# Kernel tuning notes

Measured on AMD Instinct MI355X. Metric: run time of the kernel, lower is better.

## Reference

```python
import jax, jax.numpy as jnp
import numpy as np

PAD = 0
B, P, ENC = 64, 196, 2048
L, V, H, E, A = 20, 32000, 512, 512, 512


def setup_inputs() -> dict:
    key = jax.random.key(0)
    ks = jax.random.split(key, 24)
    enc_out = jax.random.normal(ks[0], (B, P, ENC), dtype=jnp.float32)
    # captions: random tokens in [3, V) with variable lengths in [5, L]; sample 0 has full length L
    lengths = jax.random.randint(ks[1], (B,), 5, L + 1)
    lengths = lengths.at[0].set(L)
    toks = jax.random.randint(ks[2], (B, L), 3, V)
    pos = jnp.arange(L)
    y = jnp.where(pos[None, :] < lengths[:, None], toks, PAD).astype(jnp.int64)
    s = lambda k, shp, sc: (jax.random.normal(k, shp, dtype=jnp.float32) * sc)
    return {
        "encoder_output": enc_out,
        "y_encodings": y,
        "embed_table": jax.random.uniform(ks[3], (V, E), minval=-0.1, maxval=0.1, dtype=jnp.float32),
        "enc2att_W": s(ks[4], (A, ENC), 0.02),
        "hidden2att_W": s(ks[5], (A, H), 0.04),
        "att_W": s(ks[6], (1, A), 0.06),
        "att_b": jnp.zeros((1,), jnp.float32),
        "f_beta_W": s(ks[7], (ENC, H), 0.03),
        "f_beta_b": jnp.zeros((ENC,), jnp.float32),
        "W_ih": s(ks[8], (4 * H, E + ENC), 0.02),
        "b_ih": jnp.zeros((4 * H,), jnp.float32),
        "W_hh": s(ks[9], (4 * H, H), 0.04),
        "b_hh": jnp.zeros((4 * H,), jnp.float32),
        "fc_W": jax.random.uniform(ks[10], (V, H), minval=-0.1, maxval=0.1, dtype=jnp.float32),
        "fc_b": jnp.zeros((V,), jnp.float32),
        "init_h_W": s(ks[11], (H, ENC), 0.03),
        "init_h_b": jnp.zeros((H,), jnp.float32),
        "init_c_W": s(ks[12], (H, ENC), 0.03),
        "init_c_b": jnp.zeros((H,), jnp.float32),
    }


def _decode(encoder_output, y_encodings, embed_table, enc2att_W, hidden2att_W,
            att_W, att_b, f_beta_W, f_beta_b, W_ih, b_ih, W_hh, b_hh,
            fc_W, fc_b, init_h_W, init_h_b, init_c_W, init_c_b):
    # sort batch by caption length (descending), as in torch
    cap_len = jnp.sum(y_encodings != PAD, axis=1)          # [B]
    sort_idx = jnp.argsort(-cap_len)                       # stable in jax
    enc = encoder_output[sort_idx]                         # [B,P,ENC]
    caps = y_encodings[sort_idx]                           # [B,L]
    dec_len = cap_len[sort_idx] - 1                        # [B]
    T = L - 1                                              # static max decode length

    embed = embed_table[caps]                              # [B,L,E]
    mean_enc = enc.mean(axis=1)                            # [B,ENC]
    h0 = mean_enc @ init_h_W.T + init_h_b
    c0 = mean_enc @ init_c_W.T + init_c_b
    att1 = jnp.einsum('bpe,ae->bpa', enc, enc2att_W)       # [B,P,A], time-invariant

    def step(carry, xs):
        h, c = carry
        emb_t, t = xs                                      # emb_t: [B,E]
        # soft attention
        att2 = h @ hidden2att_W.T                          # [B,A]
        score = jnp.einsum('bpa,a->bp', jax.nn.relu(att1 + att2[:, None, :]), att_W[0]) + att_b[0]
        alpha = jax.nn.softmax(score, axis=1)              # [B,P]
        context = jnp.einsum('bp,bpe->be', alpha, enc)     # [B,ENC]
        gate = jax.nn.sigmoid(h @ f_beta_W.T + f_beta_b)   # [B,ENC]
        ctx = gate * context
        # LSTM cell (torch gate order: i, f, g, o)
        x_in = jnp.concatenate([emb_t, ctx], axis=1)       # [B,E+ENC]
        gates = x_in @ W_ih.T + b_ih + h @ W_hh.T + b_hh   # [B,4H]
        i_g, f_g, g_g, o_g = jnp.split(gates, 4, axis=1)
        c_new = jax.nn.sigmoid(f_g) * c + jax.nn.sigmoid(i_g) * jnp.tanh(g_g)
        h_new = jax.nn.sigmoid(o_g) * jnp.tanh(c_new)
        logits = h_new @ fc_W.T + fc_b                     # [B,V]
        active = (dec_len > t)[:, None]
        h = jnp.where(active, h_new, h)
        c = jnp.where(active, c_new, c)
        preds_t = jnp.where(active, logits, 0.0)
        alpha_t = jnp.where(active, alpha, 0.0)
        return (h, c), (preds_t, alpha_t)

    xs = (jnp.swapaxes(embed, 0, 1)[:T], jnp.arange(T))
    _, (preds, alphas) = jax.lax.scan(step, (h0, c0), xs)
    predictions = jnp.swapaxes(preds, 0, 1)               # [B,T,V]
    alphas = jnp.swapaxes(alphas, 0, 1)                   # [B,T,P]
    return predictions, alphas, dec_len, sort_idx


def reference(encoder_output, y_encodings, embed_table, enc2att_W, hidden2att_W,
              att_W, att_b, f_beta_W, f_beta_b, W_ih, b_ih, W_hh, b_hh,
              fc_W, fc_b, init_h_W, init_h_b, init_c_W, init_c_b):
    return _decode(encoder_output, y_encodings, embed_table, enc2att_W, hidden2att_W,
                   att_W, att_b, f_beta_W, f_beta_b, W_ih, b_ih, W_hh, b_hh,
                   fc_W, fc_b, init_h_W, init_h_b, init_c_W, init_c_b)
```

## Files before the change

kernel.cpp:

```cpp
#include <hip/hip_runtime.h>
#include <cstdint>
#include <cstddef>

#define BB 64
#define PE 196
#define PP 208
#define ENC 2048
#define LL 20
#define TT 19
#define VV 32000
#define HH 512
#define AA 512
#define KCAT 3072
#define XROW 3072
#define MROW 1216
#define MPAD 1280

typedef __attribute__((ext_vector_type(8))) short bf16x8;
typedef __attribute__((ext_vector_type(4))) float f32x4;
typedef unsigned short u16;
typedef unsigned int u32;

__device__ __forceinline__ float bf2f(u16 s){ return __uint_as_float(((u32)s) << 16); }
__device__ __forceinline__ u16 f2bf(float f){
  u32 u = __float_as_uint(f);
  u32 r = (u + 0x7FFFu + ((u >> 16) & 1u)) >> 16;
  return (u16)r;
}
__device__ __forceinline__ f32x4 mfma16(bf16x8 a, bf16x8 b, f32x4 c){
  return __builtin_amdgcn_mfma_f32_16x16x32_bf16(a, b, c, 0, 0, 0);
}
__device__ __forceinline__ float sigm(float x){ return 1.f / (1.f + __expf(-x)); }

__device__ __forceinline__ void gl_lds16(const u16* g, u16* l){
  __builtin_amdgcn_global_load_lds(
      (const __attribute__((address_space(1))) void*)g,
      (__attribute__((address_space(3))) void*)l, 16, 0, 0);
}


__global__ void k_sort(const int* __restrict__ y, int* __restrict__ sidx, int* __restrict__ dlen,
                       float* __restrict__ out_dlen, float* __restrict__ out_sidx){
  __shared__ int cl[BB];
  int b = threadIdx.x;
  int c = 0;
  for (int l = 0; l < LL; l++) c += (y[b*LL + l] != 0);
  cl[b] = c;
  __syncthreads();
  int r = 0;
  for (int j = 0; j < BB; j++){
    int cj = cl[j];
    r += (cj > c) || (cj == c && j < b);
  }
  sidx[r] = b; dlen[r] = c - 1;
  out_sidx[r] = (float)b; out_dlen[r] = (float)(c - 1);
}

__global__ void k_cvt(u16* __restrict__ dst, const float* __restrict__ src, int n){
  int i = blockIdx.x * blockDim.x + threadIdx.x;
  int stride = gridDim.x * blockDim.x;
  for (; i < n; i += stride) dst[i] = f2bf(src[i]);
}

__global__ void k_wcat(u16* __restrict__ wcat, const float* __restrict__ wih, const float* __restrict__ whh){
  int r = blockIdx.x;
  for (int j = threadIdx.x; j < KCAT; j += 256){
    float v = (j < 2560) ? wih[(size_t)r*2560 + j] : whh[(size_t)r*HH + (j - 2560)];
    wcat[(size_t)r*KCAT + j] = f2bf(v);
  }
}

__global__ void k_gather(u16* __restrict__ encb, const float* __restrict__ enc, const int* __restrict__ sidx){
  int b = blockIdx.x, pg = blockIdx.y;
  int s = sidx[b];
  const float* src = enc + (size_t)s * PE * ENC;
  u16* dst = encb + ((size_t)b * PP + pg * 8) * ENC;
  for (int i = threadIdx.x; i < 8 * ENC; i += 256){
    int p = pg * 8 + (i >> 11);
    dst[i] = (p < PE) ? f2bf(src[(size_t)p * ENC + (i & 2047)]) : (u16)0;
  }
}

__global__ void k_mean(float* __restrict__ mean, const u16* __restrict__ encb){
  int b = blockIdx.x;
  int e = blockIdx.y * 256 + threadIdx.x;
  const u16* p = encb + (size_t)b * PP * ENC + e;
  float s = 0.f;
#pragma unroll 14
  for (int pp = 0; pp < PE; pp++) s += bf2f(p[(size_t)pp * ENC]);
  mean[b*ENC + e] = s * (1.0f / 196.0f);
}

__global__ void k_embed(u16* __restrict__ embb, const float* __restrict__ table,
                        const int* __restrict__ y, const int* __restrict__ sidx){
  int b = blockIdx.x; int s = sidx[b];
  for (int i = threadIdx.x; i < TT * HH; i += 256){
    int tt = i >> 9, j = i & 511;
    int tok = y[s*LL + tt];
    embb[((size_t)b*TT + tt)*HH + j] = f2bf(table[(size_t)tok * HH + j]);
  }
}

__global__ void k_init(u16* __restrict__ xcat, float* __restrict__ cws, const float* __restrict__ mean,
                       const float* __restrict__ hW, const float* __restrict__ hb,
                       const float* __restrict__ cW, const float* __restrict__ cb){
  int isC = blockIdx.y;
  int col = blockIdx.x * 4 + (threadIdx.x >> 6);
  int row = threadIdx.x & 63;
  const float* W = isC ? cW : hW;
  const float4* m4 = (const float4*)(mean + (size_t)row * ENC);
  const float4* w4 = (const float4*)(W + (size_t)col * ENC);
  float acc = 0.f;
#pragma unroll 8
  for (int k = 0; k < ENC/4; k++){
    float4 a = m4[k], w = w4[k];
    acc = fmaf(a.x, w.x, acc); acc = fmaf(a.y, w.y, acc);
    acc = fmaf(a.z, w.z, acc); acc = fmaf(a.w, w.w, acc);
  }
  if (isC) cws[row*HH + col] = acc + cb[col];
  else     xcat[(size_t)row*XROW + 2560 + col] = f2bf(acc + hb[col]);
}

__global__ __launch_bounds__(256, 2) void k_att1(u16* __restrict__ att1,
                                                 const u16* __restrict__ encb,
                                                 const u16* __restrict__ e2a){
  __shared__ u16 ldsA[128 * 32];
  __shared__ u16 ldsB[128 * 32];
  int tid = threadIdx.x;
  int wave = tid >> 6, lane = tid & 63, quad = lane >> 4, l15 = lane & 15, kq = quad * 8;
  int mbase = blockIdx.x * 128;
  int nbase = blockIdx.y * 128;
  int wm = (wave >> 1) * 64, wn = (wave & 1) * 64;

  int srow = tid >> 2;
  int scol = (tid & 3) * 8;
  const u16* gA0 = encb + (size_t)(mbase + srow) * ENC + scol;
  const u16* gA1 = encb + (size_t)(mbase + 64 + srow) * ENC + scol;
  const u16* gB0 = e2a  + (size_t)(nbase + srow) * ENC + scol;
  const u16* gB1 = e2a  + (size_t)(nbase + 64 + srow) * ENC + scol;
  u16* lA0 = ldsA + tid * 8;
  u16* lA1 = ldsA + 2048 + tid * 8;
  u16* lB0 = ldsB + tid * 8;
  u16* lB1 = ldsB + 2048 + tid * 8;

  f32x4 acc[4][4] = {};
  for (int k0 = 0; k0 < ENC; k0 += 32){
    gl_lds16(gA0 + k0, lA0);
    gl_lds16(gA1 + k0, lA1);
    gl_lds16(gB0 + k0, lB0);
    gl_lds16(gB1 + k0, lB1);
    __syncthreads();
    bf16x8 af[4], bfr[4];
#pragma unroll
    for (int i = 0; i < 4; i++) af[i]  = *(const bf16x8*)(ldsA + (wm + i*16 + l15) * 32 + kq);
#pragma unroll
    for (int j = 0; j < 4; j++) bfr[j] = *(const bf16x8*)(ldsB + (wn + j*16 + l15) * 32 + kq);
#pragma unroll
    for (int i = 0; i < 4; i++)
#pragma unroll
      for (int j = 0; j < 4; j++)
        acc[i][j] = mfma16(af[i], bfr[j], acc[i][j]);
    __syncthreads();
  }
#pragma unroll
  for (int i = 0; i < 4; i++)
#pragma unroll
    for (int j = 0; j < 4; j++)
#pragma unroll
      for (int r = 0; r < 4; r++){
        int m = mbase + wm + i*16 + quad*4 + r;
        int n = nbase + wn + j*16 + l15;
        att1[(size_t)m * AA + n] = f2bf(acc[i][j][r]);
      }
}


__global__ void k_hmat(float* __restrict__ att2, float* __restrict__ gatelin,
                       const u16* __restrict__ xcat, const u16* __restrict__ whcat){
  int lane = threadIdx.x, quad = lane >> 4, l15 = lane & 15, kq = quad * 8;
  int n = blockIdx.x * 16 + l15;
  const u16* bp = whcat + (size_t)n * HH + kq;
  f32x4 acc[4] = {};
#pragma unroll 4
  for (int k0 = 0; k0 < HH; k0 += 32){
    bf16x8 bv = *(const bf16x8*)(bp + k0);
#pragma unroll
    for (int mt = 0; mt < 4; mt++){
      bf16x8 av = *(const bf16x8*)(xcat + (size_t)(mt*16 + l15)*XROW + 2560 + kq + k0);
      acc[mt] = mfma16(av, bv, acc[mt]);
    }
  }
#pragma unroll
  for (int mt = 0; mt < 4; mt++)
#pragma unroll
    for (int r = 0; r < 4; r++){
      int m = mt*16 + quad*4 + r;
      float v = acc[mt][r];
      if (n < HH) att2[m*HH + n] = v;
      else        gatelin[m*ENC + (n - HH)] = v;
    }
}

__global__ void k_score(float* __restrict__ out_alph, float* __restrict__ alpha_ws,
                        const u16* __restrict__ att1, const float* __restrict__ att2,
                        const float* __restrict__ attW, const float* __restrict__ attb,
                        const int* __restrict__ dlen, int t){
  __shared__ float a2s[AA], aws[AA], red[256];
  int b = blockIdx.x, tid = threadIdx.x;
  float* oa = out_alph + ((size_t)b*TT + t) * PE;
  if (dlen[b] <= t){
    if (tid < PE) oa[tid] = 0.f;
    return;
  }
  a2s[tid] = att2[b*AA + tid]; a2s[tid+256] = att2[b*AA + tid + 256];
  aws[tid] = attW[tid];        aws[tid+256] = attW[tid + 256];
  __syncthreads();
  float sc = -3.4e38f;
  if (tid < PE){
    const u16* row = att1 + ((size_t)b*PP + tid) * AA;
    float acc = 0.f;
#pragma unroll 8
    for (int a0 = 0; a0 < AA; a0 += 8){
      bf16x8 v = *(const bf16x8*)(row + a0);
#pragma unroll
      for (int j = 0; j < 8; j++){
        float x = bf2f((u16)v[j]) + a2s[a0 + j];
        acc = fmaf(fmaxf(x, 0.f), aws[a0 + j], acc);
      }
    }
    sc = acc + attb[0];
  }
  red[tid] = sc; __syncthreads();
  for (int s = 128; s > 0; s >>= 1){ if (tid < s) red[tid] = fmaxf(red[tid], red[tid+s]); __syncthreads(); }
  float mx = red[0]; __syncthreads();
  float ex = (tid < PE) ? __expf(sc - mx) : 0.f;
  red[tid] = ex; __syncthreads();
  for (int s = 128; s > 0; s >>= 1){ if (tid < s) red[tid] += red[tid+s]; __syncthreads(); }
  float inv = 1.f / red[0];
  if (tid < PE) oa[tid] = ex * inv;
  if (tid < PP) alpha_ws[b*PP + tid] = (tid < PE) ? ex * inv : 0.f;
}

__global__ void k_ctx(u16* __restrict__ xcat, const u16* __restrict__ encb,
                      const float* __restrict__ alpha_ws, const float* __restrict__ gatelin,
                      const float* __restrict__ fbb, const u16* __restrict__ embb,
                      const int* __restrict__ dlen, int t){
  int b = blockIdx.x;
  if (dlen[b] <= t) return;
  __shared__ float al[PP];
  int tid = threadIdx.x;
  if (tid < PP) al[tid] = alpha_ws[b*PP + tid];
  __syncthreads();
  int e = blockIdx.y * 256 + tid;
  const u16* ep = encb + (size_t)b*PP*ENC + e;
  float acc = 0.f;
#pragma unroll 14
  for (int p = 0; p < PE; p++) acc = fmaf(al[p], bf2f(ep[(size_t)p * ENC]), acc);
  float g = sigm(gatelin[b*ENC + e] + fbb[e]);
  xcat[(size_t)b*XROW + 512 + e] = f2bf(g * acc);
  if (blockIdx.y == 0){
    for (int j = tid; j < 512; j += 256)
      xcat[(size_t)b*XROW + j] = embb[((size_t)b*TT + t)*HH + j];
  }
}

__global__ void k_gates(u16* __restrict__ xcat, float* __restrict__ cws,
                        u16* __restrict__ hsave,
                        const u16* __restrict__ wcat,
                        const float* __restrict__ bih, const float* __restrict__ bhh,
                        const int* __restrict__ dlen, int t){
  __shared__ float red[4][16][64];
  int tid = threadIdx.x;
  int wave = tid >> 6, lane = tid & 63, quad = lane >> 4, l15 = lane & 15, kq = quad * 8;
  int col = blockIdx.x*16 + l15;
  int mb = blockIdx.y * 16;
  int kbase = wave * 768;
  const u16* ap = xcat + (size_t)(mb + l15)*XROW + kbase + kq;
  const u16* b0p = wcat + (size_t)(col)       *KCAT + kbase + kq;
  const u16* b1p = wcat + (size_t)(512 + col) *KCAT + kbase + kq;
  const u16* b2p = wcat + (size_t)(1024 + col)*KCAT + kbase + kq;
  const u16* b3p = wcat + (size_t)(1536 + col)*KCAT + kbase + kq;
  f32x4 a0 = {}, a1 = {}, a2 = {}, a3 = {};
#pragma unroll 4
  for (int k0 = 0; k0 < 768; k0 += 32){
    bf16x8 a  = *(const bf16x8*)(ap + k0);
    bf16x8 b0 = *(const bf16x8*)(b0p + k0);
    bf16x8 b1 = *(const bf16x8*)(b1p + k0);
    bf16x8 b2 = *(const bf16x8*)(b2p + k0);
    bf16x8 b3 = *(const bf16x8*)(b3p + k0);
    a0 = mfma16(a, b0, a0); a1 = mfma16(a, b1, a1);
    a2 = mfma16(a, b2, a2); a3 = mfma16(a, b3, a3);
  }
#pragma unroll
  for (int r = 0; r < 4; r++){
    red[wave][r][lane]      = a0[r];
    red[wave][4 + r][lane]  = a1[r];
    red[wave][8 + r][lane]  = a2[r];
    red[wave][12 + r][lane] = a3[r];
  }
  __syncthreads();
  if (wave == 0){
    float g0[4], g1[4], g2[4], g3[4];
#pragma unroll
    for (int r = 0; r < 4; r++){
      g0[r] = red[0][r][lane]      + red[1][r][lane]      + red[2][r][lane]      + red[3][r][lane];
      g1[r] = red[0][4+r][lane]    + red[1][4+r][lane]    + red[2][4+r][lane]    + red[3][4+r][lane];
      g2[r] = red[0][8+r][lane]    + red[1][8+r][lane]    + red[2][8+r][lane]    + red[3][8+r][lane];
      g3[r] = red[0][12+r][lane]   + red[1][12+r][lane]   + red[2][12+r][lane]   + red[3][12+r][lane];
    }
    float bi0 = bih[col]      + bhh[col];
    float bi1 = bih[512+col]  + bhh[512+col];
    float bi2 = bih[1024+col] + bhh[1024+col];
    float bi3 = bih[1536+col] + bhh[1536+col];
#pragma unroll
    for (int r = 0; r < 4; r++){
      int m = mb + quad*4 + r;
      if (dlen[m] > t){
        float gi = g0[r] + bi0, gf = g1[r] + bi1, gg = g2[r] + bi2, go = g3[r] + bi3;
        float cn = sigm(gf) * cws[m*HH + col] + sigm(gi) * tanhf(gg);
        cws[m*HH + col] = cn;
        u16 hb = f2bf(sigm(go) * tanhf(cn));
        xcat[(size_t)m*XROW + 2560 + col] = hb;
        hsave[((size_t)m*TT + t)*HH + col] = hb;
      }
    }
  }
}

__global__ __launch_bounds__(256, 2) void k_fcall(float* __restrict__ out,
                                                  const u16* __restrict__ hsave,
                                                  const u16* __restrict__ fcw,
                                                  const float* __restrict__ fcb,
                                                  const int* __restrict__ dlen){
  __shared__ u16 ldsA[128 * 32];
  __shared__ u16 ldsB[128 * 32];
  int tid = threadIdx.x;
  int wave = tid >> 6, lane = tid & 63, quad = lane >> 4, l15 = lane & 15, kq = quad * 8;
  int mbase = blockIdx.x * 128;
  int nbase = blockIdx.y * 128;
  int wm = (wave >> 1) * 64, wn = (wave & 1) * 64;

  int srow = tid >> 2;
  int scol = (tid & 3) * 8;
  const u16* gA0 = hsave + (size_t)(mbase + srow) * HH + scol;
  const u16* gA1 = hsave + (size_t)(mbase + 64 + srow) * HH + scol;
  const u16* gB0 = fcw + (size_t)(nbase + srow) * HH + scol;
  const u16* gB1 = fcw + (size_t)(nbase + 64 + srow) * HH + scol;
  u16* lA0 = ldsA + tid * 8;
  u16* lA1 = ldsA + 2048 + tid * 8;
  u16* lB0 = ldsB + tid * 8;
  u16* lB1 = ldsB + 2048 + tid * 8;

  f32x4 acc[4][4] = {};
  for (int k0 = 0; k0 < HH; k0 += 32){
    gl_lds16(gA0 + k0, lA0);
    gl_lds16(gA1 + k0, lA1);
    gl_lds16(gB0 + k0, lB0);
    gl_lds16(gB1 + k0, lB1);
    __syncthreads();
    bf16x8 af[4], bfr[4];
#pragma unroll
    for (int i = 0; i < 4; i++) af[i]  = *(const bf16x8*)(ldsA + (wm + i*16 + l15) * 32 + kq);
#pragma unroll
    for (int j = 0; j < 4; j++) bfr[j] = *(const bf16x8*)(ldsB + (wn + j*16 + l15) * 32 + kq);
#pragma unroll
    for (int i = 0; i < 4; i++)
#pragma unroll
      for (int j = 0; j < 4; j++)
        acc[i][j] = mfma16(af[i], bfr[j], acc[i][j]);
    __syncthreads();
  }
#pragma unroll
  for (int i = 0; i < 4; i++)
#pragma unroll
    for (int r = 0; r < 4; r++){
      int m = mbase + wm + i*16 + quad*4 + r;
      if (m < MROW){
        int b = m / TT, t = m - b*TT;
        bool act = dlen[b] > t;
        float* op = out + (size_t)m * VV + nbase + wn + l15;
#pragma unroll
        for (int j = 0; j < 4; j++){
          int n = nbase + wn + j*16 + l15;
          op[j*16] = act ? (acc[i][j][r] + fcb[n]) : 0.f;
        }
      }
    }
}

extern "C" void kernel_launch(void* const* d_in, const int* in_sizes, int n_in,
                              void* d_out, int out_size, void* d_ws, size_t ws_size,
                              hipStream_t stream){
  const float* enc  = (const float*)d_in[0];
  const int*   y    = (const int*)  d_in[1];
  const float* etab = (const float*)d_in[2];
  const float* e2aW = (const float*)d_in[3];
  const float* h2aW = (const float*)d_in[4];
  const float* attW = (const float*)d_in[5];
  const float* attb = (const float*)d_in[6];
  const float* fbW  = (const float*)d_in[7];
  const float* fbb  = (const float*)d_in[8];
  const float* wih  = (const float*)d_in[9];
  const float* bih  = (const float*)d_in[10];
  const float* whh  = (const float*)d_in[11];
  const float* bhh  = (const float*)d_in[12];
  const float* fcW  = (const float*)d_in[13];
  const float* fcb  = (const float*)d_in[14];
  const float* ihW  = (const float*)d_in[15];
  const float* ihb  = (const float*)d_in[16];
  const float* icW  = (const float*)d_in[17];
  const float* icb  = (const float*)d_in[18];

  char* ws = (char*)d_ws;
  size_t off = 0;
  auto alloc = [&](size_t bytes){ void* p = ws + off; off += (bytes + 255) & ~(size_t)255; return p; };
  u16* encb    = (u16*)alloc((size_t)BB*PP*ENC*2);
  u16* att1    = (u16*)alloc((size_t)BB*PP*AA*2);
  u16* fcwb    = (u16*)alloc((size_t)VV*HH*2);
  u16* wcat    = (u16*)alloc((size_t)2048*KCAT*2);
  u16* whcat   = (u16*)alloc((size_t)2560*HH*2);
  u16* e2ab    = (u16*)alloc((size_t)AA*ENC*2);
  u16* embb    = (u16*)alloc((size_t)BB*TT*HH*2);
  u16* xcat    = (u16*)alloc((size_t)BB*XROW*2);
  u16* hsave   = (u16*)alloc((size_t)MPAD*HH*2);
  float* att2  = (float*)alloc((size_t)BB*AA*4);
  float* gatel = (float*)alloc((size_t)BB*ENC*4);
  float* alphw = (float*)alloc((size_t)BB*PP*4);
  float* cws   = (float*)alloc((size_t)BB*HH*4);
  float* mean  = (float*)alloc((size_t)BB*ENC*4);
  int* sidx    = (int*)alloc(BB*4);
  int* dlen    = (int*)alloc(BB*4);

  float* out      = (float*)d_out;
  float* out_alph = out + (size_t)BB*TT*VV;
  float* out_dlen = out_alph + (size_t)BB*TT*PE;
  float* out_sidx = out_dlen + BB;

  k_sort<<<1, 64, 0, stream>>>(y, sidx, dlen, out_dlen, out_sidx);
  k_cvt<<<2048, 256, 0, stream>>>(e2ab, e2aW, AA*ENC);
  k_cvt<<<2048, 256, 0, stream>>>(whcat, h2aW, AA*HH);
  k_cvt<<<2048, 256, 0, stream>>>(whcat + (size_t)AA*HH, fbW, ENC*HH);
  k_cvt<<<2048, 256, 0, stream>>>(fcwb, fcW, VV*HH);
  k_wcat<<<2048, 256, 0, stream>>>(wcat, wih, whh);
  k_gather<<<dim3(64, 26), 256, 0, stream>>>(encb, enc, sidx);
  k_mean<<<dim3(64, 8), 256, 0, stream>>>(mean, encb);
  k_embed<<<64, 256, 0, stream>>>(embb, etab, y, sidx);
  k_init<<<dim3(128, 2), 256, 0, stream>>>(xcat, cws, mean, ihW, ihb, icW, icb);
  k_att1<<<dim3(104, 4), 256, 0, stream>>>(att1, encb, e2ab);

  for (int t = 0; t < TT; t++){
    k_hmat<<<160, 64, 0, stream>>>(att2, gatel, xcat, whcat);
    k_score<<<64, 256, 0, stream>>>(out_alph, alphw, att1, att2, attW, attb, dlen, t);
    k_ctx<<<dim3(64, 8), 256, 0, stream>>>(xcat, encb, alphw, gatel, fbb, embb, dlen, t);
    k_gates<<<dim3(32, 4), 256, 0, stream>>>(xcat, cws, hsave, wcat, bih, bhh, dlen, t);
  }
  k_fcall<<<dim3(MPAD/128, VV/128), 256, 0, stream>>>(out, hsave, fcwb, fcb, dlen);
}
```

Measured before the change: 1.663 ms.

## Fuse attention score and context kernels; remap FC workgroups across XCDs

Merges the per-step score/softmax kernel and the context kernel into one launch per batch row. The alpha weights now stay in shared memory instead of going through a workspace buffer. Scores are computed one pixel per wave with coalesced vector loads and a shuffle reduction, and the context sum uses 8-wide bf16 vector loads per thread. The cost is that context now runs on only 64 workgroups instead of 512, which lowers parallelism on the encoder read. The final FC GEMM switches to a 1D grid with an XCD-aware block remap to improve L2 locality.

```diff
diff --git a/kernel.cpp b/kernel.cpp
--- a/kernel.cpp
+++ b/kernel.cpp
@@ -201,35 +201,49 @@
     }
 }
 
-__global__ void k_score(float* __restrict__ out_alph, float* __restrict__ alpha_ws,
-                        const u16* __restrict__ att1, const float* __restrict__ att2,
-                        const float* __restrict__ attW, const float* __restrict__ attb,
-                        const int* __restrict__ dlen, int t){
-  __shared__ float a2s[AA], aws[AA], red[256];
+__global__ __launch_bounds__(256) void k_sctx(
+    float* __restrict__ out_alph, u16* __restrict__ xcat,
+    const u16* __restrict__ att1, const float* __restrict__ att2,
+    const float* __restrict__ attW, const float* __restrict__ attb,
+    const u16* __restrict__ encb, const float* __restrict__ gatelin,
+    const float* __restrict__ fbb, const u16* __restrict__ embb,
+    const int* __restrict__ dlen, int t){
   int b = blockIdx.x, tid = threadIdx.x;
+  int wave = tid >> 6, lane = tid & 63;
   float* oa = out_alph + ((size_t)b*TT + t) * PE;
   if (dlen[b] <= t){
     if (tid < PE) oa[tid] = 0.f;
     return;
   }
-  a2s[tid] = att2[b*AA + tid]; a2s[tid+256] = att2[b*AA + tid + 256];
-  aws[tid] = attW[tid];        aws[tid+256] = attW[tid + 256];
+  __shared__ float sc_s[PP];
+  __shared__ float al[PP];
+  __shared__ float red[256];
+
+  float a2r[8], awr[8];
+  {
+    const float4* a2p = (const float4*)(att2 + b*AA + lane*8);
+    const float4* awp = (const float4*)(attW + lane*8);
+    float4 x0 = a2p[0], x1 = a2p[1], w0 = awp[0], w1 = awp[1];
+    a2r[0]=x0.x; a2r[1]=x0.y; a2r[2]=x0.z; a2r[3]=x0.w;
+    a2r[4]=x1.x; a2r[5]=x1.y; a2r[6]=x1.z; a2r[7]=x1.w;
+    awr[0]=w0.x; awr[1]=w0.y; awr[2]=w0.z; awr[3]=w0.w;
+    awr[4]=w1.x; awr[5]=w1.y; awr[6]=w1.z; awr[7]=w1.w;
+  }
+  float ab0 = attb[0];
+  for (int p = wave; p < PE; p += 4){
+    bf16x8 v = *(const bf16x8*)(att1 + ((size_t)b*PP + p)*AA + lane*8);
+    float acc = 0.f;
+#pragma unroll
+    for (int j = 0; j < 8; j++){
+      float x = bf2f((u16)v[j]) + a2r[j];
+      acc = fmaf(fmaxf(x, 0.f), awr[j], acc);
+    }
+#pragma unroll
+    for (int s = 32; s > 0; s >>= 1) acc += __shfl_xor(acc, s);
+    if (lane == 0) sc_s[p] = acc + ab0;
+  }
   __syncthreads();
-  float sc = -3.4e38f;
-  if (tid < PE){
-    const u16* row = att1 + ((size_t)b*PP + tid) * AA;
-    float acc = 0.f;
-#pragma unroll 8
-    for (int a0 = 0; a0 < AA; a0 += 8){
-      bf16x8 v = *(const bf16x8*)(row + a0);
-#pragma unroll
-      for (int j = 0; j < 8; j++){
-        float x = bf2f((u16)v[j]) + a2s[a0 + j];
-        acc = fmaf(fmaxf(x, 0.f), aws[a0 + j], acc);
-      }
-    }
-    sc = acc + attb[0];
-  }
+  float sc = (tid < PE) ? sc_s[tid] : -3.4e38f;
   red[tid] = sc; __syncthreads();
   for (int s = 128; s > 0; s >>= 1){ if (tid < s) red[tid] = fmaxf(red[tid], red[tid+s]); __syncthreads(); }
   float mx = red[0]; __syncthreads();
@@ -238,30 +252,30 @@
   for (int s = 128; s > 0; s >>= 1){ if (tid < s) red[tid] += red[tid+s]; __syncthreads(); }
   float inv = 1.f / red[0];
   if (tid < PE) oa[tid] = ex * inv;
-  if (tid < PP) alpha_ws[b*PP + tid] = (tid < PE) ? ex * inv : 0.f;
-}
-
-__global__ void k_ctx(u16* __restrict__ xcat, const u16* __restrict__ encb,
-                      const float* __restrict__ alpha_ws, const float* __restrict__ gatelin,
-                      const float* __restrict__ fbb, const u16* __restrict__ embb,
-                      const int* __restrict__ dlen, int t){
-  int b = blockIdx.x;
-  if (dlen[b] <= t) return;
-  __shared__ float al[PP];
-  int tid = threadIdx.x;
-  if (tid < PP) al[tid] = alpha_ws[b*PP + tid];
+  if (tid < PP) al[tid] = (tid < PE) ? ex * inv : 0.f;
+  if (tid < 64){
+    bf16x8 ev = *(const bf16x8*)(embb + ((size_t)b*TT + t)*HH + tid*8);
+    *(bf16x8*)(xcat + (size_t)b*XROW + tid*8) = ev;
+  }
   __syncthreads();
-  int e = blockIdx.y * 256 + tid;
-  const u16* ep = encb + (size_t)b*PP*ENC + e;
-  float acc = 0.f;
-#pragma unroll 14
-  for (int p = 0; p < PE; p++) acc = fmaf(al[p], bf2f(ep[(size_t)p * ENC]), acc);
-  float g = sigm(gatelin[b*ENC + e] + fbb[e]);
-  xcat[(size_t)b*XROW + 512 + e] = f2bf(g * acc);
-  if (blockIdx.y == 0){
-    for (int j = tid; j < 512; j += 256)
-      xcat[(size_t)b*XROW + j] = embb[((size_t)b*TT + t)*HH + j];
-  }
+  const u16* ep = encb + (size_t)b*PP*ENC + tid*8;
+  float acc[8] = {};
+#pragma unroll 4
+  for (int p = 0; p < PE; p++){
+    bf16x8 v = *(const bf16x8*)(ep + (size_t)p*ENC);
+    float a = al[p];
+#pragma unroll
+    for (int j = 0; j < 8; j++) acc[j] = fmaf(a, bf2f((u16)v[j]), acc[j]);
+  }
+  const float4* glp = (const float4*)(gatelin + b*ENC + tid*8);
+  const float4* fbp = (const float4*)(fbb + tid*8);
+  float4 g0 = glp[0], g1 = glp[1], f0 = fbp[0], f1 = fbp[1];
+  float gl[8] = {g0.x,g0.y,g0.z,g0.w,g1.x,g1.y,g1.z,g1.w};
+  float fb[8] = {f0.x,f0.y,f0.z,f0.w,f1.x,f1.y,f1.z,f1.w};
+  bf16x8 cv;
+#pragma unroll
+  for (int j = 0; j < 8; j++) cv[j] = (short)f2bf(sigm(gl[j] + fb[j]) * acc[j]);
+  *(bf16x8*)(xcat + (size_t)b*XROW + 512 + tid*8) = cv;
 }
 
 __global__ void k_gates(u16* __restrict__ xcat, float* __restrict__ cws,
@@ -332,12 +346,20 @@
                                                   const u16* __restrict__ fcw,
                                                   const float* __restrict__ fcb,
                                                   const int* __restrict__ dlen){
+  const int nwg = (MPAD/128) * (VV/128);
+  const int q = nwg >> 3, r = nwg & 7;
+  int id = blockIdx.x;
+  int xcd = id & 7, local = id >> 3;
+  int wgid = (xcd < r ? xcd*(q+1) : r*(q+1) + (xcd-r)*q) + local;
+  int mt = wgid % (MPAD/128);
+  int nt = wgid / (MPAD/128);
+
   __shared__ u16 ldsA[128 * 32];
   __shared__ u16 ldsB[128 * 32];
   int tid = threadIdx.x;
   int wave = tid >> 6, lane = tid & 63, quad = lane >> 4, l15 = lane & 15, kq = quad * 8;
-  int mbase = blockIdx.x * 128;
-  int nbase = blockIdx.y * 128;
+  int mbase = mt * 128;
+  int nbase = nt * 128;
   int wm = (wave >> 1) * 64, wn = (wave & 1) * 64;
 
   int srow = tid >> 2;
@@ -373,8 +395,8 @@
 #pragma unroll
   for (int i = 0; i < 4; i++)
 #pragma unroll
-    for (int r = 0; r < 4; r++){
-      int m = mbase + wm + i*16 + quad*4 + r;
+    for (int r2 = 0; r2 < 4; r2++){
+      int m = mbase + wm + i*16 + quad*4 + r2;
       if (m < MROW){
         int b = m / TT, t = m - b*TT;
         bool act = dlen[b] > t;
@@ -382,7 +404,7 @@
 #pragma unroll
         for (int j = 0; j < 4; j++){
           int n = nbase + wn + j*16 + l15;
-          op[j*16] = act ? (acc[i][j][r] + fcb[n]) : 0.f;
+          op[j*16] = act ? (acc[i][j][r2] + fcb[n]) : 0.f;
         }
       }
     }
@@ -425,7 +447,6 @@
   u16* hsave   = (u16*)alloc((size_t)MPAD*HH*2);
   float* att2  = (float*)alloc((size_t)BB*AA*4);
   float* gatel = (float*)alloc((size_t)BB*ENC*4);
-  float* alphw = (float*)alloc((size_t)BB*PP*4);
   float* cws   = (float*)alloc((size_t)BB*HH*4);
   float* mean  = (float*)alloc((size_t)BB*ENC*4);
   int* sidx    = (int*)alloc(BB*4);
@@ -450,9 +471,9 @@
 
   for (int t = 0; t < TT; t++){
     k_hmat<<<160, 64, 0, stream>>>(att2, gatel, xcat, whcat);
-    k_score<<<64, 256, 0, stream>>>(out_alph, alphw, att1, att2, attW, attb, dlen, t);
-    k_ctx<<<dim3(64, 8), 256, 0, stream>>>(xcat, encb, alphw, gatel, fbb, embb, dlen, t);
+    k_sctx<<<64, 256, 0, stream>>>(out_alph, xcat, att1, att2, attW, attb,
+                                   encb, gatel, fbb, embb, dlen, t);
     k_gates<<<dim3(32, 4), 256, 0, stream>>>(xcat, cws, hsave, wcat, bih, bhh, dlen, t);
   }
-  k_fcall<<<dim3(MPAD/128, VV/128), 256, 0, stream>>>(out, hsave, fcwb, fcb, dlen);
-}
+  k_fcall<<<(MPAD/128)*(VV/128), 256, 0, stream>>>(out, hsave, fcwb, fcb, dlen);
+}
```

Measured after the change: 2.190 ms. +31.7%, slower.
